# Performance work log

Hardware: AMD Instinct MI355X
Metric: run time of the kernel (lower is better)

## Reference

```python
import jax, jax.numpy as jnp
import numpy as np

EMBED_DIM = 1024
K_DIM = 64
NUM_HEADS = 16


def setup_inputs() -> dict:
    key = jax.random.key(0)
    kx, kq, kk, kv, kw = jax.random.split(key, 5)
    x = jax.random.normal(kx, (4, 2048, EMBED_DIM), dtype=jnp.float32)
    # per-head weights stacked along a leading head axis (torch.randn init)
    wq = jax.random.normal(kq, (NUM_HEADS, EMBED_DIM, K_DIM), dtype=jnp.float32)
    wk = jax.random.normal(kk, (NUM_HEADS, EMBED_DIM, K_DIM), dtype=jnp.float32)
    wv = jax.random.normal(kv, (NUM_HEADS, EMBED_DIM, K_DIM), dtype=jnp.float32)
    w = jax.random.normal(kw, (NUM_HEADS * K_DIM, EMBED_DIM), dtype=jnp.float32)
    return {"x": x, "wq": wq, "wk": wk, "wv": wv, "w": w}


def reference(x, wq, wk, wv, w):
    # x: [B,S,D]; wq/wk/wv: [H,D,K]; w: [H*K, D]
    q = jnp.einsum('bsd,hdk->bhsk', x, wq)
    k = jnp.einsum('bsd,hdk->bhsk', x, wk)
    v = jnp.einsum('bsd,hdk->bhsk', x, wv)
    scale = 1.0 / jnp.sqrt(jnp.asarray(K_DIM, x.dtype))
    scores = jnp.einsum('bhsk,bhtk->bhst', q, k) * scale  # [B,H,S,S]
    attn = jax.nn.softmax(scores, axis=-1)
    ctx = jnp.einsum('bhst,bhtk->bhsk', attn, v)  # [B,H,S,K]
    B, H, S, K = ctx.shape
    # concat heads along last dim in head order (matches torch.cat of per-head outs)
    heads = jnp.transpose(ctx, (0, 2, 1, 3)).reshape(B, S, H * K)
    return jnp.matmul(heads, w)  # [B,S,D]
```

## Files before the change

### kernel.cpp

```cpp
#include <hip/hip_runtime.h>
#include <hip/hip_bf16.h>
#include <math.h>

#define EMBED 1024
#define KD 64
#define NH 16
#define SEQ 2048
#define BATCH 4
#define BH (BATCH * NH)
#define NTOK ((size_t)BH * SEQ * KD)

typedef float4 f4;
typedef unsigned short u16;
typedef __attribute__((ext_vector_type(8))) short v8s;
typedef __attribute__((ext_vector_type(4))) float v4f;

__device__ __forceinline__ u16 f2bf(float f) {
    unsigned u = __float_as_uint(f);
    unsigned r = (u + 0x7fffu + ((u >> 16) & 1u)) >> 16;
    return (u16)r;
}
__device__ __forceinline__ float bf2f(u16 h) {
    return __uint_as_float(((unsigned)h) << 16);
}

__device__ __forceinline__ void gload_lds16(const void* g, void* l) {
    __builtin_amdgcn_global_load_lds(
        (const __attribute__((address_space(1))) unsigned int*)g,
        (__attribute__((address_space(3))) unsigned int*)l, 16, 0, 0);
}

__global__ __launch_bounds__(256)
void convert_all_kernel(const float* __restrict__ x,
                        const float* __restrict__ wq, const float* __restrict__ wk,
                        const float* __restrict__ wv, const float* __restrict__ w,
                        u16* __restrict__ xh, u16* __restrict__ xl,
                        u16* __restrict__ Wth, u16* __restrict__ Wtl,
                        u16* __restrict__ OWth, u16* __restrict__ OWtl)
{
    int b = blockIdx.x;
    if (b < 8192) {
        size_t i = ((size_t)b * 256 + threadIdx.x) * 4;
        f4 v = *(const f4*)(x + i);
        u16 h0 = f2bf(v.x), h1 = f2bf(v.y), h2 = f2bf(v.z), h3 = f2bf(v.w);
        u16 l0 = f2bf(v.x - bf2f(h0)), l1 = f2bf(v.y - bf2f(h1));
        u16 l2 = f2bf(v.z - bf2f(h2)), l3 = f2bf(v.w - bf2f(h3));
        uint2 H, L;
        H.x = (unsigned)h0 | ((unsigned)h1 << 16);
        H.y = (unsigned)h2 | ((unsigned)h3 << 16);
        L.x = (unsigned)l0 | ((unsigned)l1 << 16);
        L.y = (unsigned)l2 | ((unsigned)l3 << 16);
        *(uint2*)(xh + i) = H;
        *(uint2*)(xl + i) = L;
    } else if (b < 8192 + 3072) {
        int n = b - 8192;
        int mat = n >> 10, nin = n & 1023, h = nin >> 6, c = nin & 63;
        const float* __restrict__ ws = (mat == 0) ? wq : (mat == 1) ? wk : wv;
        float sc = (mat == 0) ? (0.125f * 1.4426950408889634f) : 1.0f;
        for (int d = threadIdx.x; d < EMBED; d += 256) {
            float f = ws[((size_t)h * EMBED + d) * KD + c] * sc;
            u16 hi = f2bf(f);
            u16 lo = f2bf(f - bf2f(hi));
            Wth[(size_t)n * EMBED + d] = hi;
            Wtl[(size_t)n * EMBED + d] = lo;
        }
    } else {
        int n = b - 11264;
        for (int k = threadIdx.x; k < EMBED; k += 256) {
            float f = w[(size_t)k * EMBED + n];
            u16 hi = f2bf(f);
            u16 lo = f2bf(f - bf2f(hi));
            OWth[(size_t)n * EMBED + k] = hi;
            OWtl[(size_t)n * EMBED + k] = lo;
        }
    }
}

__global__ __launch_bounds__(256)
void qk_mfma_kernel(const u16* __restrict__ xh, const u16* __restrict__ xl,
                    const u16* __restrict__ Wth, const u16* __restrict__ Wtl,
                    u16* __restrict__ Qhi, u16* __restrict__ Qlo,
                    u16* __restrict__ Khi, u16* __restrict__ Klo)
{
    __shared__ u16 sAh[128 * 64];
    __shared__ u16 sAl[128 * 64];
    __shared__ u16 sBh[128 * 64];
    __shared__ u16 sBl[128 * 64];
    const int tid = threadIdx.x;
    const int lane = tid & 63, wid = tid >> 6;
    const int lm = lane & 15, lq = lane >> 4;
    const int wm = wid & 1, wn = wid >> 1;
    const int m0 = blockIdx.y * 128;
    const int n0 = blockIdx.x * 128;

    v4f acc[4][4];
#pragma unroll
    for (int mt = 0; mt < 4; ++mt)
#pragma unroll
        for (int nt = 0; nt < 4; ++nt)
            acc[mt][nt] = (v4f){0.f, 0.f, 0.f, 0.f};

    const int srow = wid * 32 + (lane >> 3);
    const int sblk = (lane & 7) ^ (lane >> 3);

    for (int k0 = 0; k0 < EMBED; k0 += 64) {
        __syncthreads();
#pragma unroll
        for (int i = 0; i < 4; ++i) {
            int row = srow + i * 8;
            size_t gA = (((size_t)(m0 + row)) << 10) + k0 + sblk * 8;
            size_t gB = (((size_t)(n0 + row)) << 10) + k0 + sblk * 8;
            int lo = (wid * 32 + i * 8) * 128;
            gload_lds16((const char*)xh + gA * 2, (char*)sAh + lo);
            gload_lds16((const char*)Wth + gB * 2, (char*)sBh + lo);
            gload_lds16((const char*)xl + gA * 2, (char*)sAl + lo);
            gload_lds16((const char*)Wtl + gB * 2, (char*)sBl + lo);
        }
        asm volatile("s_waitcnt vmcnt(0)" ::: "memory");
        __syncthreads();

#pragma unroll
        for (int kks = 0; kks < 2; ++kks) {
            const int ba = ((kks * 4 + lq) ^ (lm & 7)) * 8;
            v8s ah[4], bh[4], al[4], bl[4];
#pragma unroll
            for (int t = 0; t < 4; ++t) {
                int ra = wm * 64 + t * 16 + lm;
                int rb = wn * 64 + t * 16 + lm;
                ah[t] = *(const v8s*)&sAh[ra * 64 + ba];
                bh[t] = *(const v8s*)&sBh[rb * 64 + ba];
                al[t] = *(const v8s*)&sAl[ra * 64 + ba];
                bl[t] = *(const v8s*)&sBl[rb * 64 + ba];
            }
#pragma unroll
            for (int mt = 0; mt < 4; ++mt)
#pragma unroll
                for (int nt = 0; nt < 4; ++nt) {
                    acc[mt][nt] = __builtin_amdgcn_mfma_f32_16x16x32_bf16(ah[mt], bh[nt], acc[mt][nt], 0, 0, 0);
                    acc[mt][nt] = __builtin_amdgcn_mfma_f32_16x16x32_bf16(ah[mt], bl[nt], acc[mt][nt], 0, 0, 0);
                    acc[mt][nt] = __builtin_amdgcn_mfma_f32_16x16x32_bf16(al[mt], bh[nt], acc[mt][nt], 0, 0, 0);
                }
        }
    }

    const int mrow0 = m0 + wm * 64;
    const int ncol0 = n0 + wn * 64;
    const bool isQ = (n0 < 1024);
#pragma unroll
    for (int mt = 0; mt < 4; ++mt) {
        int sbase = mrow0 + mt * 16 + lq * 4;
        int bb = sbase >> 11, sB = sbase & 2047;
#pragma unroll
        for (int nt = 0; nt < 4; ++nt) {
            int nin = (ncol0 + nt * 16 + lm) & 1023;
            int h = nin >> 6, cc = nin & 63;
            int bh_ = bb * NH + h;
#pragma unroll
            for (int r = 0; r < 4; ++r) {
                int s = sB + r;
                float f = acc[mt][nt][r];
                u16 hi = f2bf(f);
                u16 lo = f2bf(f - bf2f(hi));
                if (isQ) {
                    size_t a = ((size_t)bh_ * SEQ + s) * KD + cc;
                    Qhi[a] = hi;
                    Qlo[a] = lo;
                } else {
                    int ccp = ((((cc >> 3) ^ (s & 7)) << 3) | (cc & 7));
                    size_t a = ((size_t)bh_ * SEQ + s) * KD + ccp;
                    Khi[a] = hi;
                    Klo[a] = lo;
                }
            }
        }
    }
}

__global__ __launch_bounds__(256)
void v_mfma_kernel(const u16* __restrict__ xh,
                   const u16* __restrict__ Wth,
                   u16* __restrict__ Vt)
{
    __shared__ u16 sAh[128 * 64];
    __shared__ u16 sBh[128 * 64];
    const int tid = threadIdx.x;
    const int lane = tid & 63, wid = tid >> 6;
    const int lm = lane & 15, lq = lane >> 4;
    const int wm = wid & 1, wn = wid >> 1;
    const int m0 = blockIdx.y * 128;
    const int n0g = 2048 + blockIdx.x * 128;

    v4f acc[4][4];
#pragma unroll
    for (int mt = 0; mt < 4; ++mt)
#pragma unroll
        for (int nt = 0; nt < 4; ++nt)
            acc[mt][nt] = (v4f){0.f, 0.f, 0.f, 0.f};

    const int srow = wid * 32 + (lane >> 3);
    const int sblk = (lane & 7) ^ (lane >> 3);

    for (int k0 = 0; k0 < EMBED; k0 += 64) {
        __syncthreads();
#pragma unroll
        for (int i = 0; i < 4; ++i) {
            int row = srow + i * 8;
            size_t gA = (((size_t)(m0 + row)) << 10) + k0 + sblk * 8;
            size_t gB = (((size_t)(n0g + row)) << 10) + k0 + sblk * 8;
            int lo = (wid * 32 + i * 8) * 128;
            gload_lds16((const char*)xh + gA * 2, (char*)sAh + lo);
            gload_lds16((const char*)Wth + gB * 2, (char*)sBh + lo);
        }
        asm volatile("s_waitcnt vmcnt(0)" ::: "memory");
        __syncthreads();

#pragma unroll
        for (int kks = 0; kks < 2; ++kks) {
            const int ba = ((kks * 4 + lq) ^ (lm & 7)) * 8;
            v8s ah[4], bh[4];
#pragma unroll
            for (int t = 0; t < 4; ++t) {
                int ra = wm * 64 + t * 16 + lm;
                int rb = wn * 64 + t * 16 + lm;
                ah[t] = *(const v8s*)&sAh[ra * 64 + ba];
                bh[t] = *(const v8s*)&sBh[rb * 64 + ba];
            }
#pragma unroll
            for (int mt = 0; mt < 4; ++mt)
#pragma unroll
                for (int nt = 0; nt < 4; ++nt)
                    acc[mt][nt] = __builtin_amdgcn_mfma_f32_16x16x32_bf16(ah[mt], bh[nt], acc[mt][nt], 0, 0, 0);
        }
    }

    const int mrow0 = m0 + wm * 64;
    const int ncol0 = n0g + wn * 64;
#pragma unroll
    for (int mt = 0; mt < 4; ++mt) {
        int sbase = mrow0 + mt * 16 + lq * 4;
        int bb = sbase >> 11, s = sbase & 2047;
#pragma unroll
        for (int nt = 0; nt < 4; ++nt) {
            int nin = (ncol0 + nt * 16 + lm) & 1023;
            int h = nin >> 6, cc = nin & 63;
            int bh_ = bb * NH + h;
            size_t a = ((size_t)bh_ * KD + cc) * SEQ
                     + (size_t)(((((s >> 3) ^ (cc & 7)) << 3)) | (s & 7));
            uint2 u;
            u.x = (unsigned)f2bf(acc[mt][nt][0]) | ((unsigned)f2bf(acc[mt][nt][1]) << 16);
            u.y = (unsigned)f2bf(acc[mt][nt][2]) | ((unsigned)f2bf(acc[mt][nt][3]) << 16);
            *(uint2*)(Vt + a) = u;
        }
    }
}

__global__ __launch_bounds__(512)
void attn_kernel(const u16* __restrict__ Qhi, const u16* __restrict__ Qlo,
                 const u16* __restrict__ Khi, const u16* __restrict__ Klo,
                 const u16* __restrict__ Vt,  u16* __restrict__ headsb)
{
    __shared__ u16 sKhi[64 * 64];
    __shared__ u16 sKlo[64 * 64];
    __shared__ u16 sVt[64 * 64];
    __shared__ u16 sPs[128 * 64];

    const int tid = threadIdx.x;
    const int lane = tid & 63, wid = tid >> 6;
    const int lm = lane & 15, lq = lane >> 4;
    const int psw = (lm & 7) << 3;
    const int rowbase = (wid >> 1) * 32 + (wid & 1) * 16;
    const int q0 = blockIdx.y * 128;
    const int bh = blockIdx.x;
    const int bb = bh >> 4, h = bh & 15;

    v8s qh[2], ql[2];
#pragma unroll
    for (int kk = 0; kk < 2; ++kk) {
        size_t g = ((size_t)bh * SEQ + q0 + rowbase + lm) * KD + kk * 32 + lq * 8;
        qh[kk] = *(const v8s*)(Qhi + g);
        ql[kk] = *(const v8s*)(Qlo + g);
    }

    v8s vones;
#pragma unroll
    for (int i = 0; i < 8; ++i) vones[i] = (short)0x3F80;
    const v4f z4 = (v4f){0.f, 0.f, 0.f, 0.f};

    int bpaddr[4];
#pragma unroll
    for (int r = 0; r < 4; ++r)
        bpaddr[r] = (((lane & 48) | (lq * 4 + r)) << 2);

    v4f ctx[4], lcol;
    float mrun = -INFINITY;
    lcol = (v4f){0.f, 0.f, 0.f, 0.f};
#pragma unroll
    for (int nt = 0; nt < 4; ++nt)
        ctx[nt] = (v4f){0.f, 0.f, 0.f, 0.f};

    const size_t kbase = (size_t)bh * SEQ * KD;
    const char* gKh = (const char*)(Khi + kbase);
    const char* gKl = (const char*)(Klo + kbase);
    const int ko = wid * 1024;
    const char* gV = (const char*)(Vt + ((size_t)bh * KD + wid * 8 + (lane >> 3)) * SEQ)
                   + (lane & 7) * 16;

    for (int t0 = 0; t0 < SEQ; t0 += 64) {
        __syncthreads();
        {
            int kb = t0 * 128 + ko + lane * 16;
            gload_lds16(gKh + kb, (char*)sKhi + ko);
            gload_lds16(gKl + kb, (char*)sKlo + ko);
            gload_lds16(gV + t0 * 2, (char*)sVt + ko);
        }
        asm volatile("s_waitcnt vmcnt(0)" ::: "memory");
        __syncthreads();

        v4f sc[4];
        __builtin_amdgcn_s_setprio(1);
#pragma unroll
        for (int kt = 0; kt < 4; ++kt) {
            int key = kt * 16 + lm;
            int blk = lq ^ (key & 7);
            v8s kh16 = *(const v8s*)&sKhi[key * 64 + blk * 8];
            v8s kl16 = *(const v8s*)&sKlo[key * 64 + blk * 8];
            sc[kt] = __builtin_amdgcn_mfma_f32_16x16x32_bf16(kh16, qh[0], z4, 0, 0, 0);
            sc[kt] = __builtin_amdgcn_mfma_f32_16x16x32_bf16(kl16, qh[0], sc[kt], 0, 0, 0);
            sc[kt] = __builtin_amdgcn_mfma_f32_16x16x32_bf16(kh16, ql[0], sc[kt], 0, 0, 0);
        }
#pragma unroll
        for (int kt = 0; kt < 4; ++kt) {
            int key = kt * 16 + lm;
            int blk = (4 + lq) ^ (key & 7);
            v8s kh16 = *(const v8s*)&sKhi[key * 64 + blk * 8];
            v8s kl16 = *(const v8s*)&sKlo[key * 64 + blk * 8];
            sc[kt] = __builtin_amdgcn_mfma_f32_16x16x32_bf16(kh16, qh[1], sc[kt], 0, 0, 0);
            sc[kt] = __builtin_amdgcn_mfma_f32_16x16x32_bf16(kl16, qh[1], sc[kt], 0, 0, 0);
            sc[kt] = __builtin_amdgcn_mfma_f32_16x16x32_bf16(kh16, ql[1], sc[kt], 0, 0, 0);
        }
        __builtin_amdgcn_s_setprio(0);

        float m0v = fmaxf(fmaxf(fmaxf(sc[0][0], sc[0][1]), sc[0][2]), sc[0][3]);
        float m1v = fmaxf(fmaxf(fmaxf(sc[1][0], sc[1][1]), sc[1][2]), sc[1][3]);
        float m2v = fmaxf(fmaxf(fmaxf(sc[2][0], sc[2][1]), sc[2][2]), sc[2][3]);
        float m3v = fmaxf(fmaxf(fmaxf(sc[3][0], sc[3][1]), sc[3][2]), sc[3][3]);
        float mx = fmaxf(fmaxf(fmaxf(m0v, m1v), m2v), m3v);
        mx = fmaxf(mx, __shfl_xor(mx, 16));
        mx = fmaxf(mx, __shfl_xor(mx, 32));

        if (!__all((int)(mx <= mrun + 8.f))) {
            float mold = mrun;
            float mnew = fmaxf(mold, mx);
            float a = __builtin_amdgcn_exp2f(mold - mnew);
            mrun = mnew;
#pragma unroll
            for (int r = 0; r < 4; ++r) {
                float ar = __uint_as_float(
                    __builtin_amdgcn_ds_bpermute(bpaddr[r], __float_as_uint(a)));
                lcol[r] *= ar;
#pragma unroll
                for (int nt = 0; nt < 4; ++nt)
                    ctx[nt][r] *= ar;
            }
        }

        {
            u16* pbase = &sPs[(rowbase + lm) * 64];
#pragma unroll
            for (int kt = 0; kt < 4; ++kt) {
                unsigned u0 = __float_as_uint(__builtin_amdgcn_exp2f(sc[kt][0] - mrun));
                unsigned u1 = __float_as_uint(__builtin_amdgcn_exp2f(sc[kt][1] - mrun));
                unsigned u2 = __float_as_uint(__builtin_amdgcn_exp2f(sc[kt][2] - mrun));
                unsigned u3 = __float_as_uint(__builtin_amdgcn_exp2f(sc[kt][3] - mrun));
                uint2 pk;
                pk.x = __builtin_amdgcn_perm(u1, u0, 0x07060302);
                pk.y = __builtin_amdgcn_perm(u3, u2, 0x07060302);
                *(uint2*)&pbase[(kt * 16 + lq * 4) ^ psw] = pk;
            }
        }

        __builtin_amdgcn_s_setprio(1);
#pragma unroll
        for (int kk2 = 0; kk2 < 2; ++kk2) {
            v8s a = *(const v8s*)&sPs[(rowbase + lm) * 64 + ((kk2 * 32 + lq * 8) ^ psw)];
#pragma unroll
            for (int nt = 0; nt < 4; ++nt) {
                int hd = nt * 16 + lm;
                int blk = (kk2 * 4 + lq) ^ (hd & 7);
                v8s b = *(const v8s*)&sVt[hd * 64 + blk * 8];
                ctx[nt] = __builtin_amdgcn_mfma_f32_16x16x32_bf16(a, b, ctx[nt], 0, 0, 0);
            }
            lcol = __builtin_amdgcn_mfma_f32_16x16x32_bf16(a, vones, lcol, 0, 0, 0);
        }
        __builtin_amdgcn_s_setprio(0);
    }

#pragma unroll
    for (int r = 0; r < 4; ++r) {
        int row = q0 + rowbase + lq * 4 + r;
        float inv = 1.0f / lcol[r];
        u16* dst = headsb + ((size_t)bb * SEQ + row) * EMBED + h * KD;
#pragma unroll
        for (int nt = 0; nt < 4; ++nt)
            dst[nt * 16 + lm] = f2bf(ctx[nt][r] * inv);
    }
}

__global__ __launch_bounds__(256)
void out_mfma_kernel(const u16* __restrict__ headsb,
                     const u16* __restrict__ OWth, const u16* __restrict__ OWtl,
                     float* __restrict__ out)
{
    __shared__ u16 sA[128 * 64];
    __shared__ u16 sBh[128 * 64];
    __shared__ u16 sBl[128 * 64];
    const int tid = threadIdx.x;
    const int lane = tid & 63, wid = tid >> 6;
    const int lm = lane & 15, lq = lane >> 4;
    const int wm = wid & 1, wn = wid >> 1;
    const int m0 = blockIdx.y * 128;
    const int n0 = blockIdx.x * 128;

    v4f acc[4][4];
#pragma unroll
    for (int mt = 0; mt < 4; ++mt)
#pragma unroll
        for (int nt = 0; nt < 4; ++nt)
            acc[mt][nt] = (v4f){0.f, 0.f, 0.f, 0.f};

    const int srow = wid * 32 + (lane >> 3);
    const int sblk = (lane & 7) ^ (lane >> 3);

    for (int k0 = 0; k0 < EMBED; k0 += 64) {
        __syncthreads();
#pragma unroll
        for (int i = 0; i < 4; ++i) {
            int row = srow + i * 8;
            size_t gA = (((size_t)(m0 + row)) << 10) + k0 + sblk * 8;
            size_t gB = (((size_t)(n0 + row)) << 10) + k0 + sblk * 8;
            int lo = (wid * 32 + i * 8) * 128;
            gload_lds16((const char*)headsb + gA * 2, (char*)sA + lo);
            gload_lds16((const char*)OWth + gB * 2, (char*)sBh + lo);
            gload_lds16((const char*)OWtl + gB * 2, (char*)sBl + lo);
        }
        asm volatile("s_waitcnt vmcnt(0)" ::: "memory");
        __syncthreads();

#pragma unroll
        for (int kks = 0; kks < 2; ++kks) {
            const int ba = ((kks * 4 + lq) ^ (lm & 7)) * 8;
            v8s ah[4], bh[4], bl[4];
#pragma unroll
            for (int t = 0; t < 4; ++t) {
                int ra = wm * 64 + t * 16 + lm;
                int rb = wn * 64 + t * 16 + lm;
                ah[t] = *(const v8s*)&sA[ra * 64 + ba];
                bh[t] = *(const v8s*)&sBh[rb * 64 + ba];
                bl[t] = *(const v8s*)&sBl[rb * 64 + ba];
            }
#pragma unroll
            for (int mt = 0; mt < 4; ++mt)
#pragma unroll
                for (int nt = 0; nt < 4; ++nt) {
                    acc[mt][nt] = __builtin_amdgcn_mfma_f32_16x16x32_bf16(ah[mt], bh[nt], acc[mt][nt], 0, 0, 0);
                    acc[mt][nt] = __builtin_amdgcn_mfma_f32_16x16x32_bf16(ah[mt], bl[nt], acc[mt][nt], 0, 0, 0);
                }
        }
    }

    const int mrow0 = m0 + wm * 64;
    const int ncol0 = n0 + wn * 64;
#pragma unroll
    for (int mt = 0; mt < 4; ++mt) {
        int sbase = mrow0 + mt * 16 + lq * 4;
#pragma unroll
        for (int nt = 0; nt < 4; ++nt) {
            int n = ncol0 + nt * 16 + lm;
#pragma unroll
            for (int r = 0; r < 4; ++r)
                out[(size_t)(sbase + r) * EMBED + n] = acc[mt][nt][r];
        }
    }
}

extern "C" void kernel_launch(void* const* d_in, const int* in_sizes, int n_in,
                              void* d_out, int out_size, void* d_ws, size_t ws_size,
                              hipStream_t stream) {
    const float* x  = (const float*)d_in[0];
    const float* wq = (const float*)d_in[1];
    const float* wk = (const float*)d_in[2];
    const float* wv = (const float*)d_in[3];
    const float* w  = (const float*)d_in[4];
    float* out = (float*)d_out;

    u16* Qhi = (u16*)d_ws;
    u16* Qlo = Qhi + NTOK;
    u16* Khi = Qlo + NTOK;
    u16* Klo = Khi + NTOK;
    u16* Vt  = Klo + NTOK;
    u16* xh  = Vt + NTOK;
    u16* xl  = xh + NTOK;
    u16* Wth = xl + NTOK;
    u16* Wtl = Wth + (size_t)3072 * 1024;
    u16* OWth = Wtl + (size_t)3072 * 1024;
    u16* OWtl = OWth + (size_t)1024 * 1024;
    u16* headsb = xh;

    convert_all_kernel<<<12288, 256, 0, stream>>>(x, wq, wk, wv, w,
                                                  xh, xl, Wth, Wtl, OWth, OWtl);

    dim3 gqk(16, 64);
    qk_mfma_kernel<<<gqk, 256, 0, stream>>>(xh, xl, Wth, Wtl, Qhi, Qlo, Khi, Klo);

    dim3 gv(8, 64);
    v_mfma_kernel<<<gv, 256, 0, stream>>>(xh, Wth, Vt);

    dim3 g2(BH, SEQ / 128);
    attn_kernel<<<g2, 512, 0, stream>>>(Qhi, Qlo, Khi, Klo, Vt, headsb);

    dim3 g3(8, 64);
    out_mfma_kernel<<<g3, 256, 0, stream>>>(headsb, OWth, OWtl, out);
}
```

Baseline: 429.3 us.

## Triple-buffer K tiles in LDS and load V directly to registers

The attention loop now keeps three LDS buffers for the K hi/lo tiles and prefetches two tiles ahead. It waits with vmcnt(2) instead of draining every load, and uses one barrier per iteration instead of two. V fragments are no longer staged through shared memory; each lane reads them straight from global memory into registers, using precomputed swizzled addresses. The aim is to hide global-load latency behind the MFMA work and cut LDS traffic and synchronisation. The cost is more LDS for the extra buffers, more registers for the V fragments, and uncoalesced-looking direct global reads of V.

```diff
diff --git a/kernel.cpp b/kernel.cpp
--- a/kernel.cpp
+++ b/kernel.cpp
@@ -259,9 +259,7 @@
                  const u16* __restrict__ Khi, const u16* __restrict__ Klo,
                  const u16* __restrict__ Vt,  u16* __restrict__ headsb)
 {
-    __shared__ u16 sKhi[64 * 64];
-    __shared__ u16 sKlo[64 * 64];
-    __shared__ u16 sVt[64 * 64];
+    __shared__ u16 sK[3][2][64 * 64];
     __shared__ u16 sPs[128 * 64];
 
     const int tid = threadIdx.x;
@@ -291,6 +289,16 @@
     for (int r = 0; r < 4; ++r)
         bpaddr[r] = (((lane & 48) | (lq * 4 + r)) << 2);
 
+    const u16* vbase[2][4];
+#pragma unroll
+    for (int kk2 = 0; kk2 < 2; ++kk2)
+#pragma unroll
+        for (int nt = 0; nt < 4; ++nt) {
+            int hd = nt * 16 + lm;
+            vbase[kk2][nt] = Vt + ((size_t)bh * KD + hd) * SEQ
+                           + (((kk2 * 4 + lq) ^ (hd & 7)) << 3);
+        }
+
     v4f ctx[4], lcol;
     float mrun = -INFINITY;
     lcol = (v4f){0.f, 0.f, 0.f, 0.f};
@@ -302,19 +310,35 @@
     const char* gKh = (const char*)(Khi + kbase);
     const char* gKl = (const char*)(Klo + kbase);
     const int ko = wid * 1024;
-    const char* gV = (const char*)(Vt + ((size_t)bh * KD + wid * 8 + (lane >> 3)) * SEQ)
-                   + (lane & 7) * 16;
-
+
+    auto STAGE = [&](int t0s, int buf) {
+        int kb = t0s * 128 + ko + lane * 16;
+        gload_lds16(gKh + kb, (char*)&sK[buf][0][0] + ko);
+        gload_lds16(gKl + kb, (char*)&sK[buf][1][0] + ko);
+    };
+
+    STAGE(0, 0);
+    STAGE(64, 1);
+
+    int cur = 0;
     for (int t0 = 0; t0 < SEQ; t0 += 64) {
-        __syncthreads();
-        {
-            int kb = t0 * 128 + ko + lane * 16;
-            gload_lds16(gKh + kb, (char*)sKhi + ko);
-            gload_lds16(gKl + kb, (char*)sKlo + ko);
-            gload_lds16(gV + t0 * 2, (char*)sVt + ko);
-        }
-        asm volatile("s_waitcnt vmcnt(0)" ::: "memory");
-        __syncthreads();
+        asm volatile("s_waitcnt vmcnt(2)" ::: "memory");
+        __syncthreads();
+
+        v8s vb[2][4];
+#pragma unroll
+        for (int kk2 = 0; kk2 < 2; ++kk2)
+#pragma unroll
+            for (int nt = 0; nt < 4; ++nt)
+                vb[kk2][nt] = *(const v8s*)(vbase[kk2][nt] + t0);
+
+        if (t0 + 128 < SEQ) {
+            int nb = cur + 2; if (nb >= 3) nb -= 3;
+            STAGE(t0 + 128, nb);
+        }
+
+        const u16* sKhi = &sK[cur][0][0];
+        const u16* sKlo = &sK[cur][1][0];
 
         v4f sc[4];
         __builtin_amdgcn_s_setprio(1);
@@ -384,15 +408,13 @@
         for (int kk2 = 0; kk2 < 2; ++kk2) {
             v8s a = *(const v8s*)&sPs[(rowbase + lm) * 64 + ((kk2 * 32 + lq * 8) ^ psw)];
 #pragma unroll
-            for (int nt = 0; nt < 4; ++nt) {
-                int hd = nt * 16 + lm;
-                int blk = (kk2 * 4 + lq) ^ (hd & 7);
-                v8s b = *(const v8s*)&sVt[hd * 64 + blk * 8];
-                ctx[nt] = __builtin_amdgcn_mfma_f32_16x16x32_bf16(a, b, ctx[nt], 0, 0, 0);
-            }
+            for (int nt = 0; nt < 4; ++nt)
+                ctx[nt] = __builtin_amdgcn_mfma_f32_16x16x32_bf16(a, vb[kk2][nt], ctx[nt], 0, 0, 0);
             lcol = __builtin_amdgcn_mfma_f32_16x16x32_bf16(a, vones, lcol, 0, 0, 0);
         }
         __builtin_amdgcn_s_setprio(0);
+
+        cur = (cur == 2) ? 0 : cur + 1;
     }
 
 #pragma unroll
```

Measured after the change: 467.6 us. 8.9% more time.
